# Performance work log

Hardware: AMD Instinct MI355X
Metric: run time of the kernel (lower is better)

Reference implementation:

```python
import jax, jax.numpy as jnp
import numpy as np

N_NODES = 50000


def gcn_conv(h_in, W, b, src, dst, deg_inv_sqrt):
    """PyG GCNConv with self-loops and symmetric normalization.
    out_i = sum_{j->i} d_j^{-1/2} d_i^{-1/2} (h_j W) + d_i^{-1} (h_i W) + b
    """
    h = h_in @ W  # [N, out] transform first (efficient GCN form)
    norm = deg_inv_sqrt[src] * deg_inv_sqrt[dst]  # [E]
    msg = h[src] * norm[:, None]  # [E, out] edge gather
    agg = jax.ops.segment_sum(msg, dst, num_segments=N_NODES)
    # self-loop contribution with norm d_i^{-1/2} * d_i^{-1/2}
    agg = agg + h * (deg_inv_sqrt ** 2)[:, None]
    return agg + b


def setup_inputs() -> dict:
    key = jax.random.key(0)
    ks = jax.random.split(key, 8)
    n_input, n_hidden, n_latent = 512, 96, 32
    E = 800000
    x = jax.random.normal(ks[0], (N_NODES, n_input), dtype=jnp.float32)
    edge_index = jax.random.randint(ks[1], (2, E), 0, N_NODES, dtype=jnp.int64)
    s = 0.05
    W1 = jax.random.normal(ks[2], (n_input, n_hidden), dtype=jnp.float32) * s
    b1 = jnp.zeros((n_hidden,), dtype=jnp.float32)
    W_mu = jax.random.normal(ks[3], (n_hidden, n_latent), dtype=jnp.float32) * s
    b_mu = jnp.zeros((n_latent,), dtype=jnp.float32)
    W_logstd = jax.random.normal(ks[4], (n_hidden, n_latent), dtype=jnp.float32) * s
    b_logstd = jnp.zeros((n_latent,), dtype=jnp.float32)
    return {"x": x, "W1": W1, "b1": b1, "W_mu": W_mu, "b_mu": b_mu,
            "W_logstd": W_logstd, "b_logstd": b_logstd, "edge_index": edge_index}


def reference(x, W1, b1, W_mu, b_mu, W_logstd, b_logstd, edge_index):
    src, dst = edge_index[0], edge_index[1]
    # degree from targets with self-loops (PyG gcn_norm convention)
    deg = jax.ops.segment_sum(jnp.ones_like(dst, dtype=x.dtype), dst,
                              num_segments=N_NODES) + 1.0
    deg_inv_sqrt = jax.lax.rsqrt(deg)
    hidden = jax.nn.relu(gcn_conv(x, W1, b1, src, dst, deg_inv_sqrt))
    # dropout_rate = 0.0 -> identity
    mu = gcn_conv(hidden, W_mu, b_mu, src, dst, deg_inv_sqrt)
    logstd = gcn_conv(hidden, W_logstd, b_logstd, src, dst, deg_inv_sqrt)
    return (mu, logstd)
```

## Files before the change

kernel.cpp:

```cpp
#include <hip/hip_runtime.h>

#define N_NODES 50000
#define NIN 512
#define NH 96
#define NL 32
#define NH2 64

#define NB2 196
#define NBLK 128
#define BCAP 5120

typedef __attribute__((ext_vector_type(8))) short short8v;
typedef __attribute__((ext_vector_type(4))) float f32x4;

__device__ __forceinline__ unsigned short f2bf(float f) {
    unsigned u = __float_as_uint(f);
    u = (u + 0x7FFFu + ((u >> 16) & 1u)) >> 16;
    return (unsigned short)u;
}
__device__ __forceinline__ float bf2f(unsigned short h) {
    return __uint_as_float((unsigned)h << 16);
}

__global__ __launch_bounds__(256) void k_prep(const float* __restrict__ W1,
                                              const float* __restrict__ Wmu,
                                              const float* __restrict__ Wls,
                                              unsigned short* __restrict__ WbT,
                                              unsigned short* __restrict__ W2T,
                                              int* __restrict__ gcur) {
    int idx = blockIdx.x * 256 + threadIdx.x;
    if (idx < NH * NIN) {
        int n = idx >> 9, k = idx & 511;
        WbT[idx] = f2bf(W1[(size_t)k * NH + n]);
    } else if (idx < NH * NIN + NH2 * NH) {
        int j = idx - NH * NIN;
        int n = j / NH, k = j - n * NH;
        float v = (n < NL) ? Wmu[k * NL + n] : Wls[k * NL + (n - NL)];
        W2T[j] = f2bf(v);
    }
    if (idx < NB2) gcur[idx] = 0;
}

__global__ __launch_bounds__(256) void k_coarse(const int* __restrict__ src,
                                                const int* __restrict__ dst,
                                                int* __restrict__ gcur,
                                                unsigned* __restrict__ cpair, int E) {
    __shared__ int hist[NB2];
    __shared__ int lpos[NB2];
    int t = threadIdx.x;
    int ch = (E + NBLK - 1) / NBLK;
    int e0 = blockIdx.x * ch, e1 = min(e0 + ch, E);
    for (int b = t; b < NB2; b += 256) hist[b] = 0;
    __syncthreads();
    for (int e = e0 + t; e < e1; e += 256)
        atomicAdd(&hist[dst[e] >> 8], 1);
    __syncthreads();
    for (int b = t; b < NB2; b += 256) {
        int cnt = hist[b];
        int base = (cnt > 0) ? atomicAdd(&gcur[b], cnt) : 0;
        lpos[b] = b * BCAP + base;
    }
    __syncthreads();
    for (int e = e0 + t; e < e1; e += 256) {
        int s = src[e], d = dst[e];
        int pos = atomicAdd(&lpos[d >> 8], 1);
        cpair[pos] = (unsigned)s | ((unsigned)d << 16);
    }
}

__global__ __launch_bounds__(256) void k_bscan(const int* __restrict__ gcur,
                                               int* __restrict__ bbase,
                                               int* __restrict__ rowoff) {
    __shared__ int s[256];
    int t = threadIdx.x;
    int v = (t < NB2) ? gcur[t] : 0;
    s[t] = v;
    __syncthreads();
    for (int off = 1; off < 256; off <<= 1) {
        int u = (t >= off) ? s[t - off] : 0;
        __syncthreads();
        s[t] += u;
        __syncthreads();
    }
    if (t < NB2) bbase[t] = s[t] - v;
    if (t == NB2 - 1) { bbase[NB2] = s[t]; rowoff[N_NODES] = s[t]; }
}

__global__ __launch_bounds__(256) void k_fine(const unsigned* __restrict__ cpair,
                                              const int* __restrict__ gcur,
                                              const int* __restrict__ bbase,
                                              int* __restrict__ rowoff,
                                              float* __restrict__ dis,
                                              int* __restrict__ esrc) {
    __shared__ int lcnt[256];
    __shared__ int lscan[256];
    int bb = blockIdx.x;
    int n0 = bb << 8;
    int t = threadIdx.x;
    lcnt[t] = 0;
    __syncthreads();
    int p0 = bb * BCAP;
    int p1 = p0 + gcur[bb];
    int base = bbase[bb];
    for (int p = p0 + t; p < p1; p += 256)
        atomicAdd(&lcnt[(cpair[p] >> 16) - n0], 1);
    __syncthreads();
    int cnt = lcnt[t];
    lscan[t] = cnt;
    __syncthreads();
    for (int off = 1; off < 256; off <<= 1) {
        int u = (t >= off) ? lscan[t - off] : 0;
        __syncthreads();
        lscan[t] += u;
        __syncthreads();
    }
    int excl = lscan[t] - cnt;
    int node = n0 + t;
    if (node < N_NODES) {
        rowoff[node] = base + excl;
        dis[node] = rsqrtf((float)cnt + 1.0f);
    }
    lcnt[t] = base + excl;
    __syncthreads();
    for (int p = p0 + t; p < p1; p += 256) {
        unsigned u = cpair[p];
        int d = (int)(u >> 16);
        int pos = atomicAdd(&lcnt[d - n0], 1);
        esrc[pos] = (int)(u & 0xFFFFu);
    }
}

#define GBM 64
__global__ __launch_bounds__(256, 3) void k_gemm1(const float* __restrict__ x,
                                                  const unsigned short* __restrict__ WbT,
                                                  const float* __restrict__ dis,
                                                  unsigned short* __restrict__ hb, int M) {
    __shared__ __align__(16) char lA[64 * 128];
    __shared__ __align__(16) char lB[96 * 128];
    int tid = threadIdx.x;
    int lane = tid & 63, w = tid >> 6;
    int l15 = lane & 15, hi = lane >> 4;
    int m0 = blockIdx.x * GBM;

    f32x4 acc[6];
#pragma unroll
    for (int nt = 0; nt < 6; ++nt)
#pragma unroll
        for (int i = 0; i < 4; ++i) acc[nt][i] = 0.f;

    int key = l15 & 7;
    int arow = (w * 16 + l15) * 128;

    for (int kt = 0; kt < 8; ++kt) {
        __syncthreads();
#pragma unroll
        for (int i = 0; i < 2; ++i) {
            int s = i * 256 + tid;
            int r = s >> 3, sl = s & 7;
            const float* p = x + (size_t)min(m0 + r, M - 1) * NIN + kt * 64 + sl * 8;
            float4 a0 = *reinterpret_cast<const float4*>(p);
            float4 a1 = *reinterpret_cast<const float4*>(p + 4);
            uint4 pk;
            pk.x = (unsigned)f2bf(a0.x) | ((unsigned)f2bf(a0.y) << 16);
            pk.y = (unsigned)f2bf(a0.z) | ((unsigned)f2bf(a0.w) << 16);
            pk.z = (unsigned)f2bf(a1.x) | ((unsigned)f2bf(a1.y) << 16);
            pk.w = (unsigned)f2bf(a1.z) | ((unsigned)f2bf(a1.w) << 16);
            *reinterpret_cast<uint4*>(lA + r * 128 + ((sl ^ (r & 7)) << 4)) = pk;
        }
#pragma unroll
        for (int i = 0; i < 3; ++i) {
            int s = i * 256 + tid;
            int n = s >> 3, sl = s & 7;
            uint4 bv = *reinterpret_cast<const uint4*>(WbT + (size_t)n * NIN + kt * 64 + sl * 8);
            *reinterpret_cast<uint4*>(lB + n * 128 + ((sl ^ (n & 7)) << 4)) = bv;
        }
        __syncthreads();

#pragma unroll
        for (int kc = 0; kc < 2; ++kc) {
            int off = (((kc * 4 + hi) ^ key) << 4);
            short8v a = *reinterpret_cast<const short8v*>(lA + arow + off);
#pragma unroll
            for (int nt = 0; nt < 6; ++nt) {
                short8v bv = *reinterpret_cast<const short8v*>(lB + (nt * 16 + l15) * 128 + off);
                acc[nt] = __builtin_amdgcn_mfma_f32_16x16x32_bf16(a, bv, acc[nt], 0, 0, 0);
            }
        }
    }

    int rbase = m0 + w * 16 + hi * 4;
#pragma unroll
    for (int r = 0; r < 4; ++r) {
        int orow = rbase + r;
        if (orow < M) {
            float dv = dis[orow];
            unsigned short* op = hb + (size_t)orow * NH + l15;
#pragma unroll
            for (int nt = 0; nt < 6; ++nt) op[nt * 16] = f2bf(acc[nt][r] * dv);
        }
    }
}

__global__ __launch_bounds__(256) void k_gather1(const ushort4* __restrict__ hb4,
                                                 const int* __restrict__ rowoff,
                                                 const int* __restrict__ esrc,
                                                 const float* __restrict__ dis,
                                                 const float* __restrict__ b1,
                                                 ushort4* __restrict__ hid4) {
    int tid = threadIdx.x;
    int node = blockIdx.x * 8 + (tid >> 5);
    int c = tid & 31;
    if (node >= N_NODES) return;
    int p0 = rowoff[node], p1 = rowoff[node + 1];
    bool act = (c < 24);
    float ax = 0.f, ay = 0.f, az = 0.f, aw = 0.f;
    for (int pb = p0; pb < p1; pb += 32) {
        int nb = min(32, p1 - pb);
        int sv = (c < nb) ? esrc[pb + c] : 0;
#pragma unroll 4
        for (int j = 0; j < nb; j++) {
            int s = __shfl(sv, j, 32);
            if (act) {
                ushort4 v = hb4[(size_t)s * 24 + c];
                ax += bf2f(v.x); ay += bf2f(v.y); az += bf2f(v.z); aw += bf2f(v.w);
            }
        }
    }
    if (act) {
        float dv = dis[node];
        ushort4 hv = hb4[(size_t)node * 24 + c];
        float4 bv = reinterpret_cast<const float4*>(b1)[c];
        ushort4 o;
        o.x = f2bf(fmaxf((ax + bf2f(hv.x)) * dv + bv.x, 0.f));
        o.y = f2bf(fmaxf((ay + bf2f(hv.y)) * dv + bv.y, 0.f));
        o.z = f2bf(fmaxf((az + bf2f(hv.z)) * dv + bv.z, 0.f));
        o.w = f2bf(fmaxf((aw + bf2f(hv.w)) * dv + bv.w, 0.f));
        hid4[(size_t)node * 24 + c] = o;
    }
}

#define GBM2 64
__global__ __launch_bounds__(256) void k_gemm2(const unsigned short* __restrict__ hid,
                                               const unsigned short* __restrict__ W2T,
                                               const float* __restrict__ dis,
                                               unsigned short* __restrict__ h23, int M) {
    __shared__ __align__(16) char lA[64 * 256];
    __shared__ __align__(16) char lB[64 * 256];
    int tid = threadIdx.x;
    int lane = tid & 63, w = tid >> 6;
    int l15 = lane & 15, hi = lane >> 4;
    int m0 = blockIdx.x * GBM2;

#pragma unroll
    for (int i = 0; i < 3; ++i) {
        int s = i * 256 + tid;
        int r = s / 12, sl = s - r * 12;
        uint4 v = *reinterpret_cast<const uint4*>(
            hid + (size_t)min(m0 + r, M - 1) * NH + sl * 8);
        *reinterpret_cast<uint4*>(lA + r * 256 + ((sl ^ (r & 7)) << 4)) = v;
    }
#pragma unroll
    for (int i = 0; i < 3; ++i) {
        int s = i * 256 + tid;
        int n = s / 12, sl = s - n * 12;
        uint4 v = *reinterpret_cast<const uint4*>(W2T + (size_t)n * NH + sl * 8);
        *reinterpret_cast<uint4*>(lB + n * 256 + ((sl ^ (n & 7)) << 4)) = v;
    }
    __syncthreads();

    f32x4 acc[4];
#pragma unroll
    for (int nt = 0; nt < 4; ++nt)
#pragma unroll
        for (int i = 0; i < 4; ++i) acc[nt][i] = 0.f;

    int key = l15 & 7;
    const char* aptr = lA + (w * 16 + l15) * 256;
#pragma unroll
    for (int kc = 0; kc < 3; ++kc) {
        int off = (((kc * 4 + hi) ^ key) << 4);
        short8v a = *reinterpret_cast<const short8v*>(aptr + off);
#pragma unroll
        for (int nt = 0; nt < 4; ++nt) {
            short8v bv = *reinterpret_cast<const short8v*>(lB + (nt * 16 + l15) * 256 + off);
            acc[nt] = __builtin_amdgcn_mfma_f32_16x16x32_bf16(a, bv, acc[nt], 0, 0, 0);
        }
    }

    int rbase = m0 + w * 16 + hi * 4;
#pragma unroll
    for (int r = 0; r < 4; ++r) {
        int orow = rbase + r;
        if (orow < M) {
            float dv = dis[orow];
            unsigned short* op = h23 + (size_t)orow * NH2 + l15;
#pragma unroll
            for (int nt = 0; nt < 4; ++nt) op[nt * 16] = f2bf(acc[nt][r] * dv);
        }
    }
}

__global__ __launch_bounds__(256) void k_gather2(const ushort4* __restrict__ hb4,
                                                 const int* __restrict__ rowoff,
                                                 const int* __restrict__ esrc,
                                                 const float* __restrict__ dis,
                                                 const float* __restrict__ bmu,
                                                 const float* __restrict__ bls,
                                                 float4* __restrict__ out4) {
    int tid = threadIdx.x;
    int node = blockIdx.x * 16 + (tid >> 4);
    int c = tid & 15;
    if (node >= N_NODES) return;
    int p0 = rowoff[node], p1 = rowoff[node + 1];
    float ax = 0.f, ay = 0.f, az = 0.f, aw = 0.f;
    for (int pb = p0; pb < p1; pb += 16) {
        int nb = min(16, p1 - pb);
        int sv = (c < nb) ? esrc[pb + c] : 0;
#pragma unroll 4
        for (int j = 0; j < nb; j++) {
            int s = __shfl(sv, j, 16);
            ushort4 v = hb4[(size_t)s * 16 + c];
            ax += bf2f(v.x); ay += bf2f(v.y); az += bf2f(v.z); aw += bf2f(v.w);
        }
    }
    float dv = dis[node];
    ushort4 hv = hb4[(size_t)node * 16 + c];
    float4 bv = (c < 8) ? reinterpret_cast<const float4*>(bmu)[c]
                        : reinterpret_cast<const float4*>(bls)[c - 8];
    float4 o;
    o.x = (ax + bf2f(hv.x)) * dv + bv.x;
    o.y = (ay + bf2f(hv.y)) * dv + bv.y;
    o.z = (az + bf2f(hv.z)) * dv + bv.z;
    o.w = (aw + bf2f(hv.w)) * dv + bv.w;
    if (c < 8) out4[(size_t)node * 8 + c] = o;
    else       out4[(size_t)N_NODES * 8 + (size_t)node * 8 + (c - 8)] = o;
}

extern "C" void kernel_launch(void* const* d_in, const int* in_sizes, int n_in,
                              void* d_out, int out_size, void* d_ws, size_t ws_size,
                              hipStream_t stream) {
    const float* x   = (const float*)d_in[0];
    const float* W1  = (const float*)d_in[1];
    const float* b1  = (const float*)d_in[2];
    const float* Wmu = (const float*)d_in[3];
    const float* bmu = (const float*)d_in[4];
    const float* Wls = (const float*)d_in[5];
    const float* bls = (const float*)d_in[6];
    const int*   ei  = (const int*)d_in[7];
    int E = in_sizes[7] / 2;
    const int* src  = ei;
    const int* dstp = ei + E;

    char* w = (char*)d_ws;
    int* rowoff  = (int*)w;            w += ((size_t)N_NODES + 4) * 4;
    float* dis   = (float*)w;          w += (size_t)N_NODES * 4;
    int* bbase   = (int*)w;            w += ((size_t)NB2 + 4) * 4;
    int* gcur    = (int*)w;            w += ((size_t)NB2 + 4) * 4;
    int* esrc    = (int*)w;            w += (size_t)E * 4;
    unsigned* cpair = (unsigned*)w;    w += (size_t)NB2 * BCAP * 4;
    unsigned short* WbT  = (unsigned short*)w;  w += (size_t)NH * NIN * 2;
    unsigned short* W2T  = (unsigned short*)w;  w += (size_t)NH2 * NH * 2;
    unsigned short* hbuf = (unsigned short*)w;  w += (size_t)N_NODES * NH * 2;
    unsigned short* hid  = (unsigned short*)w;  w += (size_t)N_NODES * NH * 2;
    unsigned short* h23  = (unsigned short*)w;  w += (size_t)N_NODES * NH2 * 2;

    int prep_n = NH * NIN + NH2 * NH;
    k_prep<<<(prep_n + 255) / 256, 256, 0, stream>>>(W1, Wmu, Wls, WbT, W2T, gcur);

    k_coarse<<<NBLK, 256, 0, stream>>>(src, dstp, gcur, cpair, E);
    k_bscan<<<1, 256, 0, stream>>>(gcur, bbase, rowoff);
    k_fine<<<NB2, 256, 0, stream>>>(cpair, gcur, bbase, rowoff, dis, esrc);

    k_gemm1<<<(N_NODES + GBM - 1) / GBM, 256, 0, stream>>>(x, WbT, dis, hbuf, N_NODES);

    k_gather1<<<(N_NODES + 7) / 8, 256, 0, stream>>>(
        (const ushort4*)hbuf, rowoff, esrc, dis, b1, (ushort4*)hid);

    k_gemm2<<<(N_NODES + GBM2 - 1) / GBM2, 256, 0, stream>>>(hid, W2T, dis, h23, N_NODES);

    k_gather2<<<(N_NODES + 15) / 16, 256, 0, stream>>>(
        (const ushort4*)h23, rowoff, esrc, dis, bmu, bls, (float4*)d_out);
}
```

Measured before the change: 142.3 us.

## Fuse layer-1 gather into layer-2 GEMM and fold block scan into fine pass

The layer-1 neighbour aggregation (with bias and ReLU) now writes its bf16 hidden rows straight into the LDS A-tile of the second GEMM, so the hidden matrix never goes to global memory and one launch is saved. The separate single-block bucket scan is removed; each fine-sort block computes its own base offset by reducing the preceding bucket counts. The float-to-bf16 conversion also switches to the HIP library intrinsic. In exchange, the fused kernel has fewer blocks, each doing 8 serial gathers per warp group, which reduces latency hiding, and every fine block repeats a small reduction.

```diff
diff --git a/kernel.cpp b/kernel.cpp
--- a/kernel.cpp
+++ b/kernel.cpp
@@ -1,4 +1,5 @@
 #include <hip/hip_runtime.h>
+#include <hip/hip_bf16.h>
 
 #define N_NODES 50000
 #define NIN 512
@@ -14,9 +15,10 @@
 typedef __attribute__((ext_vector_type(4))) float f32x4;
 
 __device__ __forceinline__ unsigned short f2bf(float f) {
-    unsigned u = __float_as_uint(f);
-    u = (u + 0x7FFFu + ((u >> 16) & 1u)) >> 16;
-    return (unsigned short)u;
+    __hip_bfloat16 h = __float2bfloat16(f);
+    unsigned short u;
+    __builtin_memcpy(&u, &h, 2);
+    return u;
 }
 __device__ __forceinline__ float bf2f(unsigned short h) {
     return __uint_as_float((unsigned)h << 16);
@@ -68,27 +70,8 @@
     }
 }
 
-__global__ __launch_bounds__(256) void k_bscan(const int* __restrict__ gcur,
-                                               int* __restrict__ bbase,
-                                               int* __restrict__ rowoff) {
-    __shared__ int s[256];
-    int t = threadIdx.x;
-    int v = (t < NB2) ? gcur[t] : 0;
-    s[t] = v;
-    __syncthreads();
-    for (int off = 1; off < 256; off <<= 1) {
-        int u = (t >= off) ? s[t - off] : 0;
-        __syncthreads();
-        s[t] += u;
-        __syncthreads();
-    }
-    if (t < NB2) bbase[t] = s[t] - v;
-    if (t == NB2 - 1) { bbase[NB2] = s[t]; rowoff[N_NODES] = s[t]; }
-}
-
 __global__ __launch_bounds__(256) void k_fine(const unsigned* __restrict__ cpair,
                                               const int* __restrict__ gcur,
-                                              const int* __restrict__ bbase,
                                               int* __restrict__ rowoff,
                                               float* __restrict__ dis,
                                               int* __restrict__ esrc) {
@@ -97,11 +80,18 @@
     int bb = blockIdx.x;
     int n0 = bb << 8;
     int t = threadIdx.x;
+    lscan[t] = (t < bb) ? gcur[t] : 0;
+    __syncthreads();
+    for (int off = 128; off > 0; off >>= 1) {
+        if (t < off) lscan[t] += lscan[t + off];
+        __syncthreads();
+    }
+    int base = lscan[0];
+    if (bb == NB2 - 1 && t == 0) rowoff[N_NODES] = base + gcur[bb];
     lcnt[t] = 0;
     __syncthreads();
     int p0 = bb * BCAP;
     int p1 = p0 + gcur[bb];
-    int base = bbase[bb];
     for (int p = p0 + t; p < p1; p += 256)
         atomicAdd(&lcnt[(cpair[p] >> 16) - n0], 1);
     __syncthreads();
@@ -201,64 +191,20 @@
     }
 }
 
-__global__ __launch_bounds__(256) void k_gather1(const ushort4* __restrict__ hb4,
-                                                 const int* __restrict__ rowoff,
-                                                 const int* __restrict__ esrc,
-                                                 const float* __restrict__ dis,
-                                                 const float* __restrict__ b1,
-                                                 ushort4* __restrict__ hid4) {
-    int tid = threadIdx.x;
-    int node = blockIdx.x * 8 + (tid >> 5);
-    int c = tid & 31;
-    if (node >= N_NODES) return;
-    int p0 = rowoff[node], p1 = rowoff[node + 1];
-    bool act = (c < 24);
-    float ax = 0.f, ay = 0.f, az = 0.f, aw = 0.f;
-    for (int pb = p0; pb < p1; pb += 32) {
-        int nb = min(32, p1 - pb);
-        int sv = (c < nb) ? esrc[pb + c] : 0;
-#pragma unroll 4
-        for (int j = 0; j < nb; j++) {
-            int s = __shfl(sv, j, 32);
-            if (act) {
-                ushort4 v = hb4[(size_t)s * 24 + c];
-                ax += bf2f(v.x); ay += bf2f(v.y); az += bf2f(v.z); aw += bf2f(v.w);
-            }
-        }
-    }
-    if (act) {
-        float dv = dis[node];
-        ushort4 hv = hb4[(size_t)node * 24 + c];
-        float4 bv = reinterpret_cast<const float4*>(b1)[c];
-        ushort4 o;
-        o.x = f2bf(fmaxf((ax + bf2f(hv.x)) * dv + bv.x, 0.f));
-        o.y = f2bf(fmaxf((ay + bf2f(hv.y)) * dv + bv.y, 0.f));
-        o.z = f2bf(fmaxf((az + bf2f(hv.z)) * dv + bv.z, 0.f));
-        o.w = f2bf(fmaxf((aw + bf2f(hv.w)) * dv + bv.w, 0.f));
-        hid4[(size_t)node * 24 + c] = o;
-    }
-}
-
-#define GBM2 64
-__global__ __launch_bounds__(256) void k_gemm2(const unsigned short* __restrict__ hid,
-                                               const unsigned short* __restrict__ W2T,
-                                               const float* __restrict__ dis,
-                                               unsigned short* __restrict__ h23, int M) {
+#define FB 64
+__global__ __launch_bounds__(256) void k_g1g2(const ushort4* __restrict__ hb4,
+                                              const int* __restrict__ rowoff,
+                                              const int* __restrict__ esrc,
+                                              const float* __restrict__ dis,
+                                              const float* __restrict__ b1,
+                                              const unsigned short* __restrict__ W2T,
+                                              unsigned short* __restrict__ h23, int M) {
     __shared__ __align__(16) char lA[64 * 256];
     __shared__ __align__(16) char lB[64 * 256];
     int tid = threadIdx.x;
-    int lane = tid & 63, w = tid >> 6;
-    int l15 = lane & 15, hi = lane >> 4;
-    int m0 = blockIdx.x * GBM2;
-
-#pragma unroll
-    for (int i = 0; i < 3; ++i) {
-        int s = i * 256 + tid;
-        int r = s / 12, sl = s - r * 12;
-        uint4 v = *reinterpret_cast<const uint4*>(
-            hid + (size_t)min(m0 + r, M - 1) * NH + sl * 8);
-        *reinterpret_cast<uint4*>(lA + r * 256 + ((sl ^ (r & 7)) << 4)) = v;
-    }
+    int g = tid >> 5, c = tid & 31;
+    int m0 = blockIdx.x * FB;
+
 #pragma unroll
     for (int i = 0; i < 3; ++i) {
         int s = i * 256 + tid;
@@ -266,28 +212,63 @@
         uint4 v = *reinterpret_cast<const uint4*>(W2T + (size_t)n * NH + sl * 8);
         *reinterpret_cast<uint4*>(lB + n * 256 + ((sl ^ (n & 7)) << 4)) = v;
     }
-    __syncthreads();
-
+
+    bool act = (c < 24);
+    float4 bv4 = act ? reinterpret_cast<const float4*>(b1)[c]
+                     : make_float4(0.f, 0.f, 0.f, 0.f);
+
+    for (int it = 0; it < 8; ++it) {
+        int node = m0 + g * 8 + it;
+        int nd = min(node, M - 1);
+        int p0 = rowoff[nd], p1 = rowoff[nd + 1];
+        float ax = 0.f, ay = 0.f, az = 0.f, aw = 0.f;
+        for (int pb = p0; pb < p1; pb += 32) {
+            int nb = min(32, p1 - pb);
+            int sv = (c < nb) ? esrc[pb + c] : 0;
+#pragma unroll 4
+            for (int j = 0; j < nb; j++) {
+                int s = __shfl(sv, j, 32);
+                if (act) {
+                    ushort4 v = hb4[(size_t)s * 24 + c];
+                    ax += bf2f(v.x); ay += bf2f(v.y); az += bf2f(v.z); aw += bf2f(v.w);
+                }
+            }
+        }
+        if (act) {
+            float dv = dis[nd];
+            ushort4 hv = hb4[(size_t)nd * 24 + c];
+            ushort4 o;
+            o.x = f2bf(fmaxf((ax + bf2f(hv.x)) * dv + bv4.x, 0.f));
+            o.y = f2bf(fmaxf((ay + bf2f(hv.y)) * dv + bv4.y, 0.f));
+            o.z = f2bf(fmaxf((az + bf2f(hv.z)) * dv + bv4.z, 0.f));
+            o.w = f2bf(fmaxf((aw + bf2f(hv.w)) * dv + bv4.w, 0.f));
+            int r = g * 8 + it;
+            int sl = c >> 1;
+            *reinterpret_cast<ushort4*>(
+                lA + r * 256 + (((sl ^ (r & 7))) << 4) + (c & 1) * 8) = o;
+        }
+    }
+    __syncthreads();
+
+    int lane = tid & 63, w4 = tid >> 6;
+    int l15 = lane & 15, hi = lane >> 4, key = l15 & 7;
     f32x4 acc[4];
 #pragma unroll
     for (int nt = 0; nt < 4; ++nt)
 #pragma unroll
         for (int i = 0; i < 4; ++i) acc[nt][i] = 0.f;
-
-    int key = l15 & 7;
-    const char* aptr = lA + (w * 16 + l15) * 256;
+    const char* aptr = lA + (w4 * 16 + l15) * 256;
 #pragma unroll
     for (int kc = 0; kc < 3; ++kc) {
         int off = (((kc * 4 + hi) ^ key) << 4);
         short8v a = *reinterpret_cast<const short8v*>(aptr + off);
 #pragma unroll
         for (int nt = 0; nt < 4; ++nt) {
-            short8v bv = *reinterpret_cast<const short8v*>(lB + (nt * 16 + l15) * 256 + off);
-            acc[nt] = __builtin_amdgcn_mfma_f32_16x16x32_bf16(a, bv, acc[nt], 0, 0, 0);
-        }
-    }
-
-    int rbase = m0 + w * 16 + hi * 4;
+            short8v bb = *reinterpret_cast<const short8v*>(lB + (nt * 16 + l15) * 256 + off);
+            acc[nt] = __builtin_amdgcn_mfma_f32_16x16x32_bf16(a, bb, acc[nt], 0, 0, 0);
+        }
+    }
+    int rbase = m0 + w4 * 16 + hi * 4;
 #pragma unroll
     for (int r = 0; r < 4; ++r) {
         int orow = rbase + r;
@@ -354,29 +335,24 @@
     char* w = (char*)d_ws;
     int* rowoff  = (int*)w;            w += ((size_t)N_NODES + 4) * 4;
     float* dis   = (float*)w;          w += (size_t)N_NODES * 4;
-    int* bbase   = (int*)w;            w += ((size_t)NB2 + 4) * 4;
     int* gcur    = (int*)w;            w += ((size_t)NB2 + 4) * 4;
     int* esrc    = (int*)w;            w += (size_t)E * 4;
     unsigned* cpair = (unsigned*)w;    w += (size_t)NB2 * BCAP * 4;
     unsigned short* WbT  = (unsigned short*)w;  w += (size_t)NH * NIN * 2;
     unsigned short* W2T  = (unsigned short*)w;  w += (size_t)NH2 * NH * 2;
     unsigned short* hbuf = (unsigned short*)w;  w += (size_t)N_NODES * NH * 2;
-    unsigned short* hid  = (unsigned short*)w;  w += (size_t)N_NODES * NH * 2;
     unsigned short* h23  = (unsigned short*)w;  w += (size_t)N_NODES * NH2 * 2;
 
     int prep_n = NH * NIN + NH2 * NH;
     k_prep<<<(prep_n + 255) / 256, 256, 0, stream>>>(W1, Wmu, Wls, WbT, W2T, gcur);
 
     k_coarse<<<NBLK, 256, 0, stream>>>(src, dstp, gcur, cpair, E);
-    k_bscan<<<1, 256, 0, stream>>>(gcur, bbase, rowoff);
-    k_fine<<<NB2, 256, 0, stream>>>(cpair, gcur, bbase, rowoff, dis, esrc);
+    k_fine<<<NB2, 256, 0, stream>>>(cpair, gcur, rowoff, dis, esrc);
 
     k_gemm1<<<(N_NODES + GBM - 1) / GBM, 256, 0, stream>>>(x, WbT, dis, hbuf, N_NODES);
 
-    k_gather1<<<(N_NODES + 7) / 8, 256, 0, stream>>>(
-        (const ushort4*)hbuf, rowoff, esrc, dis, b1, (ushort4*)hid);
-
-    k_gemm2<<<(N_NODES + GBM2 - 1) / GBM2, 256, 0, stream>>>(hid, W2T, dis, h23, N_NODES);
+    k_g1g2<<<(N_NODES + FB - 1) / FB, 256, 0, stream>>>(
+        (const ushort4*)hbuf, rowoff, esrc, dis, b1, W2T, h23, N_NODES);
 
     k_gather2<<<(N_NODES + 15) / 16, 256, 0, stream>>>(
         (const ushort4*)h23, rowoff, esrc, dis, bmu, bls, (float4*)d_out);
```

Measured after the change: 169.4 us. 1.19x slower.
